# Optimization experiments

Hardware: AMD Instinct MI355X
Metric: run time of the kernel (lower is better)

The kernel has to match this reference:

```python
import math
import jax, jax.numpy as jnp
import numpy as np

B, C, H, W = 8, 512, 32, 32
NUM_HEADS = 8
HEAD_DIM = C // NUM_HEADS


def setup_inputs() -> dict:
    key = jax.random.key(0)
    ks = jax.random.split(key, 5)
    scale = 1.0 / math.sqrt(C)
    return {
        "x": jax.random.normal(ks[0], (B, C, H, W), dtype=jnp.float32),
        "Wq": jax.random.normal(ks[1], (C, C), dtype=jnp.float32) * scale,
        "bq": jnp.zeros((C,), dtype=jnp.float32),
        "Wk": jax.random.normal(ks[2], (C, C), dtype=jnp.float32) * scale,
        "bk": jnp.zeros((C,), dtype=jnp.float32),
        "Wv": jax.random.normal(ks[3], (C, C), dtype=jnp.float32) * scale,
        "bv": jnp.zeros((C,), dtype=jnp.float32),
        "Wo": jax.random.normal(ks[4], (C, C), dtype=jnp.float32) * scale,
        "bo": jnp.zeros((C,), dtype=jnp.float32),
    }


def reference(x, Wq, bq, Wk, bk, Wv, bv, Wo, bo):
    b, c, h, w = x.shape
    t = h * w
    # (B,C,H,W) -> (B,T,C) token sequence
    xt = x.reshape(b, c, t).transpose(0, 2, 1)
    Q = xt @ Wq + bq
    K = xt @ Wk + bk
    V = xt @ Wv + bv
    # (B,T,C) -> (B,nh,T,hd)
    def split_heads(z):
        return z.reshape(b, t, NUM_HEADS, HEAD_DIM).transpose(0, 2, 1, 3)
    Qh, Kh, Vh = split_heads(Q), split_heads(K), split_heads(V)
    S = jnp.einsum("bhqd,bhkd->bhqk", Qh, Kh) / math.sqrt(HEAD_DIM)
    A = jax.nn.softmax(S, axis=-1)  # dropout p=0.0 -> identity
    Y = jnp.einsum("bhqk,bhkd->bhqd", A, Vh)
    Y = Y.transpose(0, 2, 1, 3).reshape(b, t, c)
    O = Y @ Wo + bo
    out = xt + O
    return out.transpose(0, 2, 1).reshape(b, c, h, w)
```

## Files before the change

kernel.cpp:

```cpp
#include <hip/hip_runtime.h>
#include <hip/hip_bf16.h>

#define B_  8
#define C_  512
#define T_  1024
#define NH_ 8
#define HD_ 64

#define QSCALE 0.1803368801111243f

using short8 = __attribute__((ext_vector_type(8))) short;
using f32x4  = __attribute__((ext_vector_type(4))) float;
using us4    = __attribute__((ext_vector_type(4))) unsigned short;
using u32x2  = __attribute__((ext_vector_type(2))) unsigned int;

__device__ __forceinline__ unsigned short f2bf(float f) {
    unsigned u = __builtin_bit_cast(unsigned, f);
    u += 0x7fff + ((u >> 16) & 1);
    return (unsigned short)(u >> 16);
}
__device__ __forceinline__ unsigned pack2bf(float lo, float hi) {
    __hip_bfloat162 h = __float22bfloat162_rn(float2{lo, hi});
    unsigned u;
    __builtin_memcpy(&u, &h, 4);
    return u;
}

__device__ __forceinline__ void gload_lds16(const ushort* g, ushort* l) {
    __builtin_amdgcn_global_load_lds(
        (const __attribute__((address_space(1))) void*)g,
        (__attribute__((address_space(3))) void*)l, 16, 0, 0);
}

__global__ __launch_bounds__(256) void k_transpose_x(const float* __restrict__ x,
                                                     ushort* __restrict__ xt) {
    __shared__ float tile[32][33];
    int b = blockIdx.z, t0 = blockIdx.x * 32, c0 = blockIdx.y * 32;
    int tx = threadIdx.x & 31, ty = threadIdx.x >> 5;
#pragma unroll
    for (int i = 0; i < 4; i++)
        tile[ty + i * 8][tx] = x[((size_t)b * C_ + c0 + ty + i * 8) * T_ + t0 + tx];
    __syncthreads();
#pragma unroll
    for (int i = 0; i < 4; i++)
        xt[((size_t)b * T_ + t0 + ty + i * 8) * C_ + c0 + tx] = f2bf(tile[tx][ty + i * 8]);
}

__global__ __launch_bounds__(256) void k_transpose_w(const float* __restrict__ Wq,
                                                     const float* __restrict__ Wk,
                                                     const float* __restrict__ Wv,
                                                     const float* __restrict__ Wo,
                                                     ushort* __restrict__ Wqkvt,
                                                     ushort* __restrict__ Wot) {
    __shared__ float tile[32][33];
    int m = blockIdx.z;
    const float* W = (m == 0) ? Wq : (m == 1) ? Wk : (m == 2) ? Wv : Wo;
    ushort* dst = (m < 3) ? (Wqkvt + (size_t)m * C_ * C_) : Wot;
    float scale = (m == 0) ? QSCALE : 1.0f;
    int k0 = blockIdx.x * 32, n0 = blockIdx.y * 32;
    int tx = threadIdx.x & 31, ty = threadIdx.x >> 5;
#pragma unroll
    for (int i = 0; i < 4; i++)
        tile[ty + i * 8][tx] = W[(size_t)(k0 + ty + i * 8) * C_ + n0 + tx];
    __syncthreads();
#pragma unroll
    for (int i = 0; i < 4; i++)
        dst[(size_t)(n0 + ty + i * 8) * C_ + k0 + tx] = f2bf(tile[tx][ty + i * 8] * scale);
}

__device__ __forceinline__ void gemm_core(const ushort* __restrict__ A,
                                          const ushort* __restrict__ Bt,
                                          int row0, int col0, int tid,
                                          ushort (*As)[8192], ushort (*Bs)[8192],
                                          f32x4 acc[4][4]) {
    f32x4 zero = {0.f, 0.f, 0.f, 0.f};
#pragma unroll
    for (int i = 0; i < 4; i++)
#pragma unroll
        for (int j = 0; j < 4; j++) acc[i][j] = zero;
    int lane = tid & 63, w = tid >> 6;
    int ql = lane & 15, g = lane >> 4;
    int wm = (w >> 1) * 64, wn = (w & 1) * 64;
    int srow = lane >> 3;
    int scol8 = (lane & 7) ^ (srow & 7);

#pragma unroll
    for (int i = 0; i < 4; i++) {
        int c = w * 4 + i;
        int r = c * 8 + srow;
        gload_lds16(A + (size_t)(row0 + r) * C_ + scol8 * 8, As[0] + c * 512);
        gload_lds16(Bt + (size_t)(col0 + r) * C_ + scol8 * 8, Bs[0] + c * 512);
    }
    __syncthreads();

    for (int kt = 0; kt < 8; kt++) {
        int cur = kt & 1;
        if (kt < 7) {
            int k0 = (kt + 1) * 64;
#pragma unroll
            for (int i = 0; i < 4; i++) {
                int c = w * 4 + i;
                int r = c * 8 + srow;
                gload_lds16(A + (size_t)(row0 + r) * C_ + k0 + scol8 * 8, As[cur ^ 1] + c * 512);
                gload_lds16(Bt + (size_t)(col0 + r) * C_ + k0 + scol8 * 8, Bs[cur ^ 1] + c * 512);
            }
        }
        const ushort* Ac = As[cur];
        const ushort* Bc = Bs[cur];
        __builtin_amdgcn_s_setprio(1);
#pragma unroll
        for (int s = 0; s < 2; s++) {
            short8 a[4], b[4];
            int cs = ((4 * s + g) ^ (ql & 7)) * 8;
#pragma unroll
            for (int mt = 0; mt < 4; mt++)
                a[mt] = *(const short8*)(Ac + (wm + mt * 16 + ql) * 64 + cs);
#pragma unroll
            for (int nt = 0; nt < 4; nt++)
                b[nt] = *(const short8*)(Bc + (wn + nt * 16 + ql) * 64 + cs);
#pragma unroll
            for (int mt = 0; mt < 4; mt++)
#pragma unroll
                for (int nt = 0; nt < 4; nt++)
                    acc[mt][nt] = __builtin_amdgcn_mfma_f32_16x16x32_bf16(
                        a[mt], b[nt], acc[mt][nt], 0, 0, 0);
        }
        __builtin_amdgcn_s_setprio(0);
        __syncthreads();
    }
}

__global__ __launch_bounds__(256) void k_qkv(const ushort* __restrict__ xt,
                                             const ushort* __restrict__ Wqkvt,
                                             const float* __restrict__ bq,
                                             const float* __restrict__ bk,
                                             const float* __restrict__ bv,
                                             ushort* __restrict__ Qh,
                                             ushort* __restrict__ Kh,
                                             ushort* __restrict__ Vt) {
    __shared__ __align__(16) ushort As[2][8192];
    __shared__ __align__(16) ushort Bs[2][8192];
    f32x4 acc[4][4];
    int tid = threadIdx.x;
    int row0 = blockIdx.x * 128, col0 = blockIdx.y * 128;
    gemm_core(xt, Wqkvt, row0, col0, tid, As, Bs, acc);
    int lane = tid & 63, w = tid >> 6;
    int wm = (w >> 1) * 64, wn = (w & 1) * 64;
    int which = col0 >> 9;
    const float* bias = (which == 0) ? bq : (which == 1) ? bk : bv;
    float bscale = (which == 0) ? QSCALE : 1.0f;
#pragma unroll
    for (int mt = 0; mt < 4; mt++) {
        int grow0 = row0 + wm + mt * 16 + ((lane >> 4) << 2);
        int b = grow0 >> 10, t = grow0 & 1023;
#pragma unroll
        for (int nt = 0; nt < 4; nt++) {
            int gcol = col0 + wn + nt * 16 + (lane & 15);
            int hc = gcol & 511;
            float bsv = bias[hc] * bscale;
            int h = hc >> 6, d = hc & 63;
            if (which == 2) {
                us4 pk;
#pragma unroll
                for (int r = 0; r < 4; r++) pk[r] = f2bf(acc[mt][nt][r] + bsv);
                *(us4*)(Vt + ((size_t)(b * NH_ + h) * HD_ + d) * T_ + t) = pk;
            } else {
                ushort* dst = (which == 0) ? Qh : Kh;
#pragma unroll
                for (int r = 0; r < 4; r++)
                    dst[((size_t)(b * NH_ + h) * T_ + t + r) * HD_ + d] =
                        f2bf(acc[mt][nt][r] + bsv);
            }
        }
    }
}

__global__ __launch_bounds__(512) void k_attn(const ushort* __restrict__ Qh,
                                              const ushort* __restrict__ Kh,
                                              const ushort* __restrict__ Vt,
                                              ushort* __restrict__ Y) {
    __shared__ __align__(16) ushort Ks[2][64 * 64];
    __shared__ __align__(16) ushort Vs[2][64 * 64];
    __shared__ __align__(16) ushort Pws[8][16 * 64];
    int tid = threadIdx.x, lane = tid & 63, w = tid >> 6;
    int g = lane >> 4, ql = lane & 15;
    int bh = blockIdx.x & 63, q0 = (blockIdx.x >> 6) * 128;
    int b = bh >> 3, h = bh & 7;
    ushort* Pw = Pws[w];
    int srow = lane >> 3;
    int scol8 = (lane & 7) ^ (srow & 7);
    const ushort* Kbase = Kh + (size_t)bh * T_ * HD_;
    const ushort* Vbase = Vt + (size_t)bh * HD_ * T_;

    short8 qa[2];
#pragma unroll
    for (int s = 0; s < 2; s++)
        qa[s] = *(const short8*)(Qh + ((size_t)bh * T_ + q0 + w * 16 + ql) * HD_ + s * 32 + g * 8);

    short8 ones;
    {
        short ov = (ql == 0) ? (short)0x3F80 : (short)0;
#pragma unroll
        for (int j = 0; j < 8; j++) ones[j] = ov;
    }

    f32x4 o[4], o5;
    f32x4 zero = {0.f, 0.f, 0.f, 0.f};
#pragma unroll
    for (int i = 0; i < 4; i++) o[i] = zero;
    o5 = zero;

    {
        int r = w * 8 + srow;
        gload_lds16(Kbase + (size_t)r * HD_ + scol8 * 8, Ks[0] + w * 512);
        gload_lds16(Vbase + (size_t)r * T_ + scol8 * 8, Vs[0] + w * 512);
    }
    __syncthreads();

    for (int t = 0; t < 16; t++) {
        int cur = t & 1;
        const ushort* Kc = Ks[cur];
        const ushort* Vc = Vs[cur];
        if (t < 15) {
            int kv0 = (t + 1) * 64;
            int r = w * 8 + srow;
            gload_lds16(Kbase + (size_t)(kv0 + r) * HD_ + scol8 * 8, Ks[cur ^ 1] + w * 512);
            gload_lds16(Vbase + (size_t)r * T_ + kv0 + scol8 * 8, Vs[cur ^ 1] + w * 512);
        }

        f32x4 sT[4];
#pragma unroll
        for (int nt = 0; nt < 4; nt++) sT[nt] = zero;
        __builtin_amdgcn_s_setprio(1);
#pragma unroll
        for (int s = 0; s < 2; s++) {
            int cs = ((4 * s + g) ^ (ql & 7)) * 8;
#pragma unroll
            for (int nt = 0; nt < 4; nt++) {
                short8 ka = *(const short8*)(Kc + (nt * 16 + ql) * 64 + cs);
                sT[nt] = __builtin_amdgcn_mfma_f32_16x16x32_bf16(ka, qa[s], sT[nt], 0, 0, 0);
            }
        }
        __builtin_amdgcn_s_setprio(0);

#pragma unroll
        for (int nt = 0; nt < 4; nt++) {
            u32x2 pk;
            pk[0] = pack2bf(__builtin_amdgcn_exp2f(sT[nt][0]), __builtin_amdgcn_exp2f(sT[nt][1]));
            pk[1] = pack2bf(__builtin_amdgcn_exp2f(sT[nt][2]), __builtin_amdgcn_exp2f(sT[nt][3]));
            int gr = (2 * nt + (g >> 1)) ^ (ql & 7);
            *(u32x2*)(Pw + ql * 64 + gr * 8 + (g & 1) * 4) = pk;
        }

        __builtin_amdgcn_s_setprio(1);
#pragma unroll
        for (int s = 0; s < 2; s++) {
            int cs = ((4 * s + g) ^ (ql & 7)) * 8;
            short8 pa = *(const short8*)(Pw + ql * 64 + cs);
#pragma unroll
            for (int dt = 0; dt < 4; dt++) {
                short8 vb = *(const short8*)(Vc + (dt * 16 + ql) * 64 + cs);
                o[dt] = __builtin_amdgcn_mfma_f32_16x16x32_bf16(pa, vb, o[dt], 0, 0, 0);
            }
            o5 = __builtin_amdgcn_mfma_f32_16x16x32_bf16(pa, ones, o5, 0, 0, 0);
        }
        __builtin_amdgcn_s_setprio(0);
        __syncthreads();
    }

    float li[4];
#pragma unroll
    for (int r = 0; r < 4; r++) li[r] = 1.0f / __shfl(o5[r], g * 16);
#pragma unroll
    for (int dt = 0; dt < 4; dt++)
#pragma unroll
        for (int r = 0; r < 4; r++) {
            int t = q0 + w * 16 + 4 * g + r;
            int c = h * HD_ + dt * 16 + ql;
            Y[((size_t)b * T_ + t) * C_ + c] = f2bf(o[dt][r] * li[r]);
        }
}

__global__ __launch_bounds__(256) void k_oproj(const ushort* __restrict__ Y,
                                               const ushort* __restrict__ Wot,
                                               const float* __restrict__ bo,
                                               const float* __restrict__ x,
                                               float* __restrict__ out) {
    __shared__ __align__(16) ushort As[2][8192];
    __shared__ __align__(16) ushort Bs[2][8192];
    f32x4 acc[4][4];
    int tid = threadIdx.x;
    int row0 = blockIdx.x * 128, col0 = blockIdx.y * 128;
    gemm_core(Y, Wot, row0, col0, tid, As, Bs, acc);
    int lane = tid & 63, w = tid >> 6;
    int wm = (w >> 1) * 64, wn = (w & 1) * 64;
#pragma unroll
    for (int mt = 0; mt < 4; mt++) {
        int grow0 = row0 + wm + mt * 16 + ((lane >> 4) << 2);
        int b = grow0 >> 10, t = grow0 & 1023;
#pragma unroll
        for (int nt = 0; nt < 4; nt++) {
            int c = col0 + wn + nt * 16 + (lane & 15);
            float bsv = bo[c];
            size_t off = ((size_t)b * C_ + c) * T_ + t;
            float4 xv = *(const float4*)(x + off);
            float4 ov;
            ov.x = acc[mt][nt][0] + xv.x + bsv;
            ov.y = acc[mt][nt][1] + xv.y + bsv;
            ov.z = acc[mt][nt][2] + xv.z + bsv;
            ov.w = acc[mt][nt][3] + xv.w + bsv;
            *(float4*)(out + off) = ov;
        }
    }
}

extern "C" void kernel_launch(void* const* d_in, const int* in_sizes, int n_in,
                              void* d_out, int out_size, void* d_ws, size_t ws_size,
                              hipStream_t stream) {
    const float* x  = (const float*)d_in[0];
    const float* Wq = (const float*)d_in[1];
    const float* bq = (const float*)d_in[2];
    const float* Wk = (const float*)d_in[3];
    const float* bk = (const float*)d_in[4];
    const float* Wv = (const float*)d_in[5];
    const float* bv = (const float*)d_in[6];
    const float* Wo = (const float*)d_in[7];
    const float* bo = (const float*)d_in[8];
    float* out = (float*)d_out;

    char* ws = (char*)d_ws;
    ushort* xt    = (ushort*)(ws + 0);
    ushort* Wqkvt = (ushort*)(ws + 8388608);
    ushort* Wot   = (ushort*)(ws + 9961472);
    ushort* Qh    = (ushort*)(ws + 10485760);
    ushort* Kh    = (ushort*)(ws + 18874368);
    ushort* Vt    = (ushort*)(ws + 27262976);
    ushort* Yw    = xt;

    k_transpose_x<<<dim3(32, 16, 8), 256, 0, stream>>>(x, xt);
    k_transpose_w<<<dim3(16, 16, 4), 256, 0, stream>>>(Wq, Wk, Wv, Wo, Wqkvt, Wot);
    k_qkv<<<dim3(64, 12), 256, 0, stream>>>(xt, Wqkvt, bq, bk, bv, Qh, Kh, Vt);
    k_attn<<<dim3(512), 512, 0, stream>>>(Qh, Kh, Vt, Yw);
    k_oproj<<<dim3(64, 4), 256, 0, stream>>>(Yw, Wot, bo, x, out);
}
```

Baseline: 79.38 us.

## Switch attention to 32x32x16 MFMA with register-resident P via permlane32 swap

Result: no change. 80.78 us (+1.8%).

```diff
diff --git a/kernel.cpp b/kernel.cpp
--- a/kernel.cpp
+++ b/kernel.cpp
@@ -11,8 +11,8 @@
 
 using short8 = __attribute__((ext_vector_type(8))) short;
 using f32x4  = __attribute__((ext_vector_type(4))) float;
+using f32x16 = __attribute__((ext_vector_type(16))) float;
 using us4    = __attribute__((ext_vector_type(4))) unsigned short;
-using u32x2  = __attribute__((ext_vector_type(2))) unsigned int;
 
 __device__ __forceinline__ unsigned short f2bf(float f) {
     unsigned u = __builtin_bit_cast(unsigned, f);
@@ -181,34 +181,25 @@
                                               ushort* __restrict__ Y) {
     __shared__ __align__(16) ushort Ks[2][64 * 64];
     __shared__ __align__(16) ushort Vs[2][64 * 64];
-    __shared__ __align__(16) ushort Pws[8][16 * 64];
     int tid = threadIdx.x, lane = tid & 63, w = tid >> 6;
-    int g = lane >> 4, ql = lane & 15;
-    int bh = blockIdx.x & 63, q0 = (blockIdx.x >> 6) * 128;
+    int hi = lane >> 5, l31 = lane & 31, l7 = lane & 7;
+    int bh = blockIdx.x & 63, q0 = (blockIdx.x >> 6) * 256;
     int b = bh >> 3, h = bh & 7;
-    ushort* Pw = Pws[w];
     int srow = lane >> 3;
-    int scol8 = (lane & 7) ^ (srow & 7);
+    int scol8 = l7 ^ (srow & 7);
     const ushort* Kbase = Kh + (size_t)bh * T_ * HD_;
     const ushort* Vbase = Vt + (size_t)bh * HD_ * T_;
 
-    short8 qa[2];
-#pragma unroll
-    for (int s = 0; s < 2; s++)
-        qa[s] = *(const short8*)(Qh + ((size_t)bh * T_ + q0 + w * 16 + ql) * HD_ + s * 32 + g * 8);
-
-    short8 ones;
-    {
-        short ov = (ql == 0) ? (short)0x3F80 : (short)0;
-#pragma unroll
-        for (int j = 0; j < 8; j++) ones[j] = ov;
-    }
-
-    f32x4 o[4], o5;
-    f32x4 zero = {0.f, 0.f, 0.f, 0.f};
-#pragma unroll
-    for (int i = 0; i < 4; i++) o[i] = zero;
-    o5 = zero;
+    short8 qa[4];
+#pragma unroll
+    for (int s = 0; s < 4; s++)
+        qa[s] = *(const short8*)(Qh + ((size_t)bh * T_ + q0 + w * 32 + l31) * HD_ +
+                                 s * 16 + hi * 8);
+
+    f32x16 o0, o1;
+#pragma unroll
+    for (int i = 0; i < 16; i++) { o0[i] = 0.f; o1[i] = 0.f; }
+    float lsum = 0.f;
 
     {
         int r = w * 8 + srow;
@@ -228,57 +219,71 @@
             gload_lds16(Vbase + (size_t)r * T_ + kv0 + scol8 * 8, Vs[cur ^ 1] + w * 512);
         }
 
-        f32x4 sT[4];
-#pragma unroll
-        for (int nt = 0; nt < 4; nt++) sT[nt] = zero;
+        f32x16 sT0, sT1;
+#pragma unroll
+        for (int i = 0; i < 16; i++) { sT0[i] = 0.f; sT1[i] = 0.f; }
         __builtin_amdgcn_s_setprio(1);
 #pragma unroll
-        for (int s = 0; s < 2; s++) {
-            int cs = ((4 * s + g) ^ (ql & 7)) * 8;
-#pragma unroll
-            for (int nt = 0; nt < 4; nt++) {
-                short8 ka = *(const short8*)(Kc + (nt * 16 + ql) * 64 + cs);
-                sT[nt] = __builtin_amdgcn_mfma_f32_16x16x32_bf16(ka, qa[s], sT[nt], 0, 0, 0);
+        for (int s = 0; s < 4; s++) {
+            int cs = ((2 * s + hi) ^ l7) * 8;
+            short8 ka0 = *(const short8*)(Kc + l31 * 64 + cs);
+            short8 ka1 = *(const short8*)(Kc + (32 + l31) * 64 + cs);
+            sT0 = __builtin_amdgcn_mfma_f32_32x32x16_bf16(ka0, qa[s], sT0, 0, 0, 0);
+            sT1 = __builtin_amdgcn_mfma_f32_32x32x16_bf16(ka1, qa[s], sT1, 0, 0, 0);
+        }
+        __builtin_amdgcn_s_setprio(0);
+
+        unsigned pkv0[8], pkv1[8];
+        float ts = 0.f;
+#pragma unroll
+        for (int i = 0; i < 8; i++) {
+            float a0 = __builtin_amdgcn_exp2f(sT0[2 * i]);
+            float a1 = __builtin_amdgcn_exp2f(sT0[2 * i + 1]);
+            float b0 = __builtin_amdgcn_exp2f(sT1[2 * i]);
+            float b1 = __builtin_amdgcn_exp2f(sT1[2 * i + 1]);
+            pkv0[i] = pack2bf(a0, a1);
+            pkv1[i] = pack2bf(b0, b1);
+            ts += (a0 + a1) + (b0 + b1);
+        }
+        lsum += ts;
+
+        __builtin_amdgcn_s_setprio(1);
+#pragma unroll
+        for (int t4 = 0; t4 < 4; t4++) {
+            const int h2 = t4 & 1;
+            unsigned c0, c1, c2v, c3v;
+            if (t4 < 2) {
+                c0 = pkv0[4 * h2 + 0]; c2v = pkv0[4 * h2 + 2];
+                c1 = pkv0[4 * h2 + 1]; c3v = pkv0[4 * h2 + 3];
+            } else {
+                c0 = pkv1[4 * h2 + 0]; c2v = pkv1[4 * h2 + 2];
+                c1 = pkv1[4 * h2 + 1]; c3v = pkv1[4 * h2 + 3];
             }
-        }
-        __builtin_amdgcn_s_setprio(0);
-
-#pragma unroll
-        for (int nt = 0; nt < 4; nt++) {
-            u32x2 pk;
-            pk[0] = pack2bf(__builtin_amdgcn_exp2f(sT[nt][0]), __builtin_amdgcn_exp2f(sT[nt][1]));
-            pk[1] = pack2bf(__builtin_amdgcn_exp2f(sT[nt][2]), __builtin_amdgcn_exp2f(sT[nt][3]));
-            int gr = (2 * nt + (g >> 1)) ^ (ql & 7);
-            *(u32x2*)(Pw + ql * 64 + gr * 8 + (g & 1) * 4) = pk;
-        }
-
-        __builtin_amdgcn_s_setprio(1);
-#pragma unroll
-        for (int s = 0; s < 2; s++) {
-            int cs = ((4 * s + g) ^ (ql & 7)) * 8;
-            short8 pa = *(const short8*)(Pw + ql * 64 + cs);
-#pragma unroll
-            for (int dt = 0; dt < 4; dt++) {
-                short8 vb = *(const short8*)(Vc + (dt * 16 + ql) * 64 + cs);
-                o[dt] = __builtin_amdgcn_mfma_f32_16x16x32_bf16(pa, vb, o[dt], 0, 0, 0);
-            }
-            o5 = __builtin_amdgcn_mfma_f32_16x16x32_bf16(pa, ones, o5, 0, 0, 0);
+            asm("v_permlane32_swap_b32 %0, %1" : "+v"(c0), "+v"(c2v));
+            asm("v_permlane32_swap_b32 %0, %1" : "+v"(c1), "+v"(c3v));
+            unsigned au[4] = {c0, c1, c2v, c3v};
+            short8 pa;
+            __builtin_memcpy(&pa, au, 16);
+            int cs = ((2 * t4 + hi) ^ l7) * 8;
+            short8 vb0 = *(const short8*)(Vc + l31 * 64 + cs);
+            short8 vb1 = *(const short8*)(Vc + (32 + l31) * 64 + cs);
+            o0 = __builtin_amdgcn_mfma_f32_32x32x16_bf16(pa, vb0, o0, 0, 0, 0);
+            o1 = __builtin_amdgcn_mfma_f32_32x32x16_bf16(pa, vb1, o1, 0, 0, 0);
         }
         __builtin_amdgcn_s_setprio(0);
         __syncthreads();
     }
 
-    float li[4];
-#pragma unroll
-    for (int r = 0; r < 4; r++) li[r] = 1.0f / __shfl(o5[r], g * 16);
-#pragma unroll
-    for (int dt = 0; dt < 4; dt++)
-#pragma unroll
-        for (int r = 0; r < 4; r++) {
-            int t = q0 + w * 16 + 4 * g + r;
-            int c = h * HD_ + dt * 16 + ql;
-            Y[((size_t)b * T_ + t) * C_ + c] = f2bf(o[dt][r] * li[r]);
-        }
+    float linv = 1.0f / (lsum + __shfl_xor(lsum, 32));
+#pragma unroll
+    for (int r = 0; r < 16; r++) {
+        int qr = (r & 3) + 8 * (r >> 2) + 4 * hi;
+        float li = __shfl(linv, qr);
+        int trow = q0 + w * 32 + qr;
+        size_t base = ((size_t)b * T_ + trow) * C_ + h * HD_;
+        Y[base + l31] = f2bf(o0[r] * li);
+        Y[base + 32 + l31] = f2bf(o1[r] * li);
+    }
 }
 
 __global__ __launch_bounds__(256) void k_oproj(const ushort* __restrict__ Y,
@@ -340,6 +345,6 @@
     k_transpose_x<<<dim3(32, 16, 8), 256, 0, stream>>>(x, xt);
     k_transpose_w<<<dim3(16, 16, 4), 256, 0, stream>>>(Wq, Wk, Wv, Wo, Wqkvt, Wot);
     k_qkv<<<dim3(64, 12), 256, 0, stream>>>(xt, Wqkvt, bq, bk, bv, Qh, Kh, Vt);
-    k_attn<<<dim3(512), 512, 0, stream>>>(Qh, Kh, Vt, Yw);
+    k_attn<<<dim3(256), 512, 0, stream>>>(Qh, Kh, Vt, Yw);
     k_oproj<<<dim3(64, 4), 256, 0, stream>>>(Yw, Wot, bo, x, out);
 }
```
